# Kernel optimization log

Measured on AMD Instinct MI355X. Metric: run time of the kernel, lower is better.

The kernel has to match this reference:

```python
import jax, jax.numpy as jnp
import numpy as np

B, S, D, H, DK, DV, DO = 2, 2048, 1024, 16, 64, 64, 1024


def setup_inputs() -> dict:
    key = jax.random.key(0)
    k0, k1, k2, k3, k4 = jax.random.split(key, 5)
    x = jax.random.normal(k0, (B, S, D), dtype=jnp.float32)
    # Stacked per-head projection weights (original uses H separate Linear(bias=False));
    # stored as [H, D, d_head] so q = x @ Wq[h] per head.
    Wq = jax.random.normal(k1, (H, D, DK), dtype=jnp.float32) * 0.02
    Wk = jax.random.normal(k2, (H, D, DK), dtype=jnp.float32) * 0.02
    Wv = jax.random.normal(k3, (H, D, DV), dtype=jnp.float32) * 0.02
    # Output projection Linear(dim_v*num_heads, dim_out, bias=False), stored [H*DV, DO]
    Wo = jax.random.normal(k4, (H * DV, DO), dtype=jnp.float32) * 0.02
    return {"x": x, "Wq": Wq, "Wk": Wk, "Wv": Wv, "Wo": Wo}


def reference(x, Wq, Wk, Wv, Wo):
    # Cross-head batched version of the per-head Python loop (same math).
    q = jnp.einsum('bsd,hde->bhse', x, Wq)  # [B,H,S,DK]
    k = jnp.einsum('bsd,hde->bhse', x, Wk)  # [B,H,S,DK]
    v = jnp.einsum('bsd,hde->bhse', x, Wv)  # [B,H,S,DV]
    scale = 1.0 / jnp.sqrt(jnp.asarray(k.shape[-1], dtype=x.dtype))
    scores = jnp.einsum('bhqe,bhke->bhqk', q, k) * scale  # [B,H,S,S]
    attn = jax.nn.softmax(scores, axis=-1)
    o = jnp.einsum('bhqk,bhke->bhqe', attn, v)  # [B,H,S,DV]
    # concat heads along feature dim (head order preserved)
    o = jnp.transpose(o, (0, 2, 1, 3)).reshape(o.shape[0], o.shape[2], -1)  # [B,S,H*DV]
    return o @ Wo  # [B,S,DO]
```

## Files before the change

### kernel.cpp

```cpp
#include <hip/hip_runtime.h>

typedef __bf16 bf16;
typedef __attribute__((ext_vector_type(8))) short short8;
typedef __attribute__((ext_vector_type(4))) short short4v;
typedef __attribute__((ext_vector_type(4))) float floatx4;

#define DEVINL __device__ __forceinline__

DEVINL void gll16(const void* g, void* l) {
  __builtin_amdgcn_global_load_lds((const __attribute__((address_space(1))) void*)g,
                                   (__attribute__((address_space(3))) void*)l, 16, 0, 0);
}

DEVINL float fast_exp2(float x) { return __builtin_amdgcn_exp2f(x); }

#define QSCALE 0.18033688011112042f

__global__ __launch_bounds__(256) void prep_all(const float* __restrict__ x,
                                                const float* __restrict__ Wq,
                                                const float* __restrict__ Wk,
                                                const float* __restrict__ Wv,
                                                const float* __restrict__ Wo,
                                                bf16* __restrict__ x_bf,
                                                bf16* __restrict__ WbigT,
                                                bf16* __restrict__ WoT) {
  __shared__ float tile[64][65];
  int bid = blockIdx.x;
  if (bid < 2048) {
    int i = (bid * 256 + threadIdx.x) * 8;
    float4 a = *(const float4*)(x + i);
    float4 b = *(const float4*)(x + i + 4);
    union { bf16 h[8]; short8 s; } u;
    u.h[0] = (bf16)a.x; u.h[1] = (bf16)a.y; u.h[2] = (bf16)a.z; u.h[3] = (bf16)a.w;
    u.h[4] = (bf16)b.x; u.h[5] = (bf16)b.y; u.h[6] = (bf16)b.z; u.h[7] = (bf16)b.w;
    *(short8*)(x_bf + i) = u.s;
    return;
  }
  int t = bid - 2048;
  int which = t >> 8;
  t &= 255;
  const float* in;
  bf16* out;
  int C, tilesC, tilesPerBatch;
  long inStride;
  if (which < 3) {
    in = which == 0 ? Wq : (which == 1 ? Wk : Wv);
    out = WbigT + (long)which * 1024 * 1024;
    C = 64; tilesC = 1; tilesPerBatch = 16; inStride = 65536;
  } else {
    in = Wo; out = WoT;
    C = 1024; tilesC = 16; tilesPerBatch = 256; inStride = 0;
  }
  int batch = t / tilesPerBatch;
  int tt = t % tilesPerBatch;
  int ri = tt / tilesC, ci = tt % tilesC;
  const float* src = in + batch * inStride;
  bf16* dst = out + batch * (long)65536 * (which < 3 ? 1 : 0);
  int tx = threadIdx.x & 63, ty = threadIdx.x >> 6;
#pragma unroll
  for (int i = 0; i < 16; i++) {
    int r = ty + i * 4;
    tile[r][tx] = src[(long)(ri * 64 + r) * C + ci * 64 + tx];
  }
  __syncthreads();
#pragma unroll
  for (int i = 0; i < 16; i++) {
    int c = ty + i * 4;
    dst[(long)(ci * 64 + c) * 1024 + ri * 64 + tx] = (bf16)tile[tx][c];
  }
}

__global__ __launch_bounds__(512, 2) void gemm256_qkv(const bf16* __restrict__ A,
                                                      const bf16* __restrict__ BT,
                                                      bf16* __restrict__ q_ws,
                                                      bf16* __restrict__ k_ws,
                                                      bf16* __restrict__ v_ws) {
  extern __shared__ char lds[];
  int swz = (blockIdx.x & 7) * 24 + (blockIdx.x >> 3);
  int bm = swz / 12, bn = swz % 12;
  int tid = threadIdx.x, lane = tid & 63, wid = tid >> 6;
  int wm = wid >> 2, wn = wid & 3;
  int ql = lane & 15, g = lane >> 4;
  int sw = (ql & 7) << 4;
  int hB = wn >> 1;
  char* ldsA = lds;
  char* ldsB = lds + 65536;

  const char* Abase = (const char*)A + (long)bm * 256 * 2048;
  const char* Bbase = (const char*)BT + (long)bn * 256 * 2048;
  int scb = ((tid & 7) * 16) ^ (((tid >> 3) & 7) << 4);

  floatx4 acc[8][4] = {};
  short8 aF[4], bF[4];

#define STG(dst0, src0, kt_, h_) do {                                              \
    _Pragma("unroll") for (int j_ = 0; j_ < 2; j_++)                               \
      gll16((src0) + (long)((h_) * 128 + j_ * 64 + (tid >> 3)) * 2048              \
                   + (kt_) * 128 + scb,                                            \
            (dst0) + ((kt_) & 1) * 32768 + (h_) * 16384 + j_ * 8192 + wid * 1024); \
  } while (0)
#define LDA(slot_, frh_, kk_) do {                                                 \
    _Pragma("unroll") for (int j_ = 0; j_ < 4; j_++)                               \
      aF[j_] = *(const short8*)(ldsA + (slot_) * 32768 + wm * 16384 +              \
               (((frh_) * 4 + j_) * 16 + ql) * 128 + (((kk_) * 64 + g * 16) ^ sw));\
  } while (0)
#define LDB(slot_, kk_) do {                                                       \
    _Pragma("unroll") for (int f_ = 0; f_ < 4; f_++)                               \
      bF[f_] = *(const short8*)(ldsB + (slot_) * 32768 + hB * 16384 +              \
               ((wn & 1) * 64 + f_ * 16 + ql) * 128 + (((kk_) * 64 + g * 16) ^ sw));\
  } while (0)
#define MFMA16(frh_) do {                                                          \
    __builtin_amdgcn_s_setprio(1);                                                 \
    _Pragma("unroll") for (int j_ = 0; j_ < 4; j_++)                               \
      _Pragma("unroll") for (int f_ = 0; f_ < 4; f_++)                             \
        acc[(frh_) * 4 + j_][f_] = __builtin_amdgcn_mfma_f32_16x16x32_bf16(        \
            aF[j_], bF[f_], acc[(frh_) * 4 + j_][f_], 0, 0, 0);                    \
    __builtin_amdgcn_s_setprio(0);                                                 \
  } while (0)
#define BAR __builtin_amdgcn_s_barrier()
#define LG0 asm volatile("s_waitcnt lgkmcnt(0)" ::: "memory")

  STG(ldsB, Bbase, 0, 0); STG(ldsB, Bbase, 0, 1);
  STG(ldsA, Abase, 0, 0); STG(ldsA, Abase, 0, 1);
  STG(ldsB, Bbase, 1, 0);

  for (int it = 0; it < 8; it++) {
    int b1 = 2 * it + 1, a2 = 2 * it + 2, b2 = 2 * it + 3;
    bool more = it < 7;
    asm volatile("s_waitcnt vmcnt(2)" ::: "memory");
    BAR;
    LDA(0, 0, 0); LDB(0, 0);
    STG(ldsA, Abase, b1, 0);
    BAR; LG0; MFMA16(0); BAR;
    LDA(0, 1, 0);
    STG(ldsA, Abase, b1, 1);
    BAR; LG0; MFMA16(1); BAR;
    LDA(0, 0, 1); LDB(0, 1);
    STG(ldsB, Bbase, b1, 1);
    BAR; LG0; MFMA16(0); BAR;
    LDA(0, 1, 1);
    if (more) STG(ldsB, Bbase, a2, 0);
    BAR; LG0; MFMA16(1); BAR;
    if (more) { asm volatile("s_waitcnt vmcnt(2)" ::: "memory"); }
    else      { asm volatile("s_waitcnt vmcnt(0)" ::: "memory"); }
    BAR;
    LDA(1, 0, 0); LDB(1, 0);
    if (more) STG(ldsB, Bbase, a2, 1);
    BAR; LG0; MFMA16(0); BAR;
    LDA(1, 1, 0);
    if (more) STG(ldsA, Abase, a2, 0);
    BAR; LG0; MFMA16(1); BAR;
    LDA(1, 0, 1); LDB(1, 1);
    if (more) STG(ldsA, Abase, a2, 1);
    BAR; LG0; MFMA16(0); BAR;
    LDA(1, 1, 1);
    if (more) STG(ldsB, Bbase, b2, 0);
    BAR; LG0; MFMA16(1); BAR;
  }
#undef STG
#undef LDA
#undef LDB
#undef MFMA16
#undef BAR
#undef LG0

  if (bn < 8) {
    bf16* dst = (bn < 4) ? q_ws : k_ws;
    float scale = (bn < 4) ? QSCALE : 1.0f;
#pragma unroll
    for (int fr = 0; fr < 8; fr++)
#pragma unroll
      for (int fc = 0; fc < 4; fc++)
#pragma unroll
        for (int i = 0; i < 4; i++) {
          int r = bm * 256 + wm * 128 + fr * 16 + g * 4 + i;
          int c = bn * 256 + wn * 64 + fc * 16 + ql;
          int b = r >> 11, s = r & 2047;
          int h = (c >> 6) & 15, e = c & 63;
          long bh = (long)b * 16 + h;
          dst[(bh * 2048 + s) * 64 + e] = (bf16)(acc[fr][fc][i] * scale);
        }
  } else {
#pragma unroll
    for (int fr = 0; fr < 8; fr++)
#pragma unroll
      for (int fc = 0; fc < 4; fc++) {
        int local_c = wn * 64 + fc * 16 + ql;
        int ls0 = wm * 128 + fr * 16 + g * 4;
        int s6 = ls0 & 63;
        int sp = (ls0 & ~63) | (s6 & 35) | ((s6 & 12) << 1) | ((s6 & 16) >> 2);
        union { bf16 hh[4]; short4v s4; } u;
#pragma unroll
        for (int i = 0; i < 4; i++) u.hh[i] = (bf16)acc[fr][fc][i];
        *(short4v*)(lds + local_c * 512 + ((sp * 2) ^ ((local_c & 7) << 4))) = u.s4;
      }
    __syncthreads();
    int b = bm >> 3;
    long sbase = (long)(bm & 7) * 256;
#pragma unroll
    for (int j = 0; j < 16; j++) {
      int local_c = wid * 32 + j * 2 + (lane >> 5);
      int chunk = lane & 31;
      int cg = bn * 256 + local_c;
      int h = (cg >> 6) & 15, e = cg & 63;
      long bh = (long)b * 16 + h;
      char* dstp = (char*)v_ws + ((bh * 64 + e) * 2048 + sbase) * 2 + chunk * 16;
      *(short8*)dstp = *(const short8*)(lds + local_c * 512 + ((chunk * 16) ^ ((local_c & 7) << 4)));
    }
  }
}

__global__ __launch_bounds__(256) void gemm_out(const bf16* __restrict__ A,
                                                const bf16* __restrict__ BT,
                                                float* __restrict__ Cout,
                                                int N, int gridN) {
  int cpx = gridDim.x >> 3;
  int swz = (blockIdx.x & 7) * cpx + (blockIdx.x >> 3);
  int bm = swz / gridN, bn = swz % gridN;
  __shared__ char lds[65536];
  int tid = threadIdx.x;
  int lane = tid & 63, wid = tid >> 6;
  int wr = wid >> 1, wc = wid & 1;
  floatx4 acc[4][4] = {};
  const char* Abase = (const char*)A + (long)bm * 128 * 2048;
  const char* Bbase = (const char*)BT + (long)bn * 128 * 2048;
  int scb = ((tid & 7) * 16) ^ (((tid >> 3) & 7) << 4);

#define OSTG(kt_) do {                                                             \
    char* la_ = lds + ((kt_) & 1) * 16384;                                         \
    char* lb_ = lds + 32768 + ((kt_) & 1) * 16384;                                 \
    _Pragma("unroll") for (int q_ = 0; q_ < 4; q_++) {                             \
      gll16(Abase + (long)(q_ * 32 + (tid >> 3)) * 2048 + (kt_) * 128 + scb,       \
            la_ + q_ * 4096 + wid * 1024);                                         \
      gll16(Bbase + (long)(q_ * 32 + (tid >> 3)) * 2048 + (kt_) * 128 + scb,       \
            lb_ + q_ * 4096 + wid * 1024);                                         \
    }                                                                              \
  } while (0)

  OSTG(0);
  for (int kt = 0; kt < 16; kt++) {
    if (kt < 15) {
      OSTG(kt + 1);
      asm volatile("s_waitcnt vmcnt(8)" ::: "memory");
    } else {
      asm volatile("s_waitcnt vmcnt(0)" ::: "memory");
    }
    __builtin_amdgcn_s_barrier();
    char* la = lds + (kt & 1) * 16384;
    char* lb = lds + 32768 + (kt & 1) * 16384;
#pragma unroll
    for (int kk = 0; kk < 2; kk++) {
      short8 a[4], b[4];
#pragma unroll
      for (int mi = 0; mi < 4; mi++) {
        int row = wr * 64 + mi * 16 + (lane & 15);
        int col = (kk * 64 + (lane >> 4) * 16) ^ ((row & 7) << 4);
        a[mi] = *(const short8*)(la + row * 128 + col);
      }
#pragma unroll
      for (int ni = 0; ni < 4; ni++) {
        int row = wc * 64 + ni * 16 + (lane & 15);
        int col = (kk * 64 + (lane >> 4) * 16) ^ ((row & 7) << 4);
        b[ni] = *(const short8*)(lb + row * 128 + col);
      }
#pragma unroll
      for (int mi = 0; mi < 4; mi++)
#pragma unroll
        for (int ni = 0; ni < 4; ni++)
          acc[mi][ni] = __builtin_amdgcn_mfma_f32_16x16x32_bf16(a[mi], b[ni], acc[mi][ni], 0, 0, 0);
    }
    __builtin_amdgcn_s_barrier();
  }
#undef OSTG

#pragma unroll
  for (int mi = 0; mi < 4; mi++)
#pragma unroll
    for (int ni = 0; ni < 4; ni++)
#pragma unroll
      for (int i = 0; i < 4; i++) {
        int r = bm * 128 + wr * 64 + mi * 16 + (lane >> 4) * 4 + i;
        int c = bn * 128 + wc * 64 + ni * 16 + (lane & 15);
        Cout[(long)r * N + c] = acc[mi][ni][i];
      }
}

__global__ __launch_bounds__(1024, 4) void attn_kernel(const bf16* __restrict__ q_ws,
                                                       const bf16* __restrict__ k_ws,
                                                       const bf16* __restrict__ v_ws,
                                                       bf16* __restrict__ obuf) {
  extern __shared__ char lds[];
  int wgid = ((blockIdx.x & 7) << 5) + (blockIdx.x >> 3);
  int qt = wgid & 7;
  int bh = wgid >> 3;
  int b = bh >> 4, h = bh & 15;
  int tid = threadIdx.x, lane = tid & 63, wid = tid >> 6;
  int grp = wid >> 3, w8 = wid & 7;
  int ql = lane & 15, g = lane >> 4;
  char* kbuf = lds + grp * 65536;
  char* vbuf = kbuf + 32768;

  const char* kbase = (const char*)k_ws + (long)bh * 2048 * 128 + (long)grp * 16 * 64 * 128;
  const char* vbase = (const char*)v_ws + (long)bh * 64 * 4096 + (long)grp * 16 * 128;

  int srow = w8 * 8 + (lane >> 3);
  int scb = ((lane & 7) * 16) ^ (((lane >> 3) & 7) << 4);

#define STAGE(t_) do {                                                              \
    gll16(kbase + ((long)(t_) * 64 + srow) * 128 + scb,                             \
          kbuf + ((t_) & 3) * 8192 + w8 * 1024);                                    \
    gll16(vbase + (long)srow * 4096 + (long)(t_) * 128 + scb,                       \
          vbuf + ((t_) & 3) * 8192 + w8 * 1024);                                    \
  } while (0)

#define WAIT2_BAR do {                                                              \
    asm volatile("s_waitcnt vmcnt(2)" ::: "memory");                                \
    __builtin_amdgcn_s_barrier();                                                   \
    asm volatile("" ::: "memory");                                                  \
  } while (0)

  int sw = (ql & 7) << 4;
  int fof0 = ql * 128 + ((g * 16) ^ sw);
  int fof1 = ql * 128 + ((64 + g * 16) ^ sw);

  const bf16* qrowL = q_ws + ((long)bh * 2048 + qt * 256 + w8 * 32 + ql) * 64 + 8 * g;
  short8 qL0 = *(const short8*)(qrowL);
  short8 qL1 = *(const short8*)(qrowL + 32);
  short8 qH0 = *(const short8*)(qrowL + 1024);
  short8 qH1 = *(const short8*)(qrowL + 1024 + 32);

  union { bf16 hh[8]; short8 s; } uo1;
#pragma unroll
  for (int i = 0; i < 8; i++) uo1.hh[i] = (bf16)1.0f;
  const short8 ones = uo1.s;

  floatx4 lL = {}, lH = {};
  floatx4 oL[4] = {}, oH[4] = {};
  floatx4 saL[4], saH[4];
  short8 pbL[2], pbH[2];

#define QKSTEP(kc) do {                                                             \
    __builtin_amdgcn_s_setprio(1);                                                  \
    _Pragma("unroll") for (int t_ = 0; t_ < 4; t_++) {                              \
      short8 kf = *(const short8*)((kc) + fof0 + t_ * 2048);                        \
      saL[t_] = __builtin_amdgcn_mfma_f32_16x16x32_bf16(kf, qL0, (floatx4){}, 0, 0, 0); \
      saH[t_] = __builtin_amdgcn_mfma_f32_16x16x32_bf16(kf, qH0, (floatx4){}, 0, 0, 0); \
    }                                                                               \
    _Pragma("unroll") for (int t_ = 0; t_ < 4; t_++) {                              \
      short8 kf = *(const short8*)((kc) + fof1 + t_ * 2048);                        \
      saL[t_] = __builtin_amdgcn_mfma_f32_16x16x32_bf16(kf, qL1, saL[t_], 0, 0, 0); \
      saH[t_] = __builtin_amdgcn_mfma_f32_16x16x32_bf16(kf, qH1, saH[t_], 0, 0, 0); \
    }                                                                               \
    __builtin_amdgcn_s_setprio(0);                                                  \
  } while (0)

#define SM_HALF(sa, pb, l_acc, o_acc) do {                                          \
    if (__builtin_expect(l_acc[0] > 1e30f, 0)) {                                    \
      const float c_ = 7.8886091e-31f;                                  \
      _Pragma("unroll") for (int t_ = 0; t_ < 4; t_++)                              \
        _Pragma("unroll") for (int i_ = 0; i_ < 4; i_++) o_acc[t_][i_] *= c_;       \
      _Pragma("unroll") for (int i_ = 0; i_ < 4; i_++) l_acc[i_] *= c_;             \
    }                                                                               \
    _Pragma("unroll") for (int kk_ = 0; kk_ < 2; kk_++) {                           \
      union { bf16 hh[8]; short8 s; } up_;                                          \
      _Pragma("unroll") for (int r_ = 0; r_ < 4; r_++)                              \
        up_.hh[r_] = (bf16)fast_exp2(sa[2 * kk_][r_]);                              \
      _Pragma("unroll") for (int r_ = 0; r_ < 4; r_++)                              \
        up_.hh[4 + r_] = (bf16)fast_exp2(sa[2 * kk_ + 1][r_]);                      \
      pb[kk_] = up_.s;                                                              \
    }                                                                               \
  } while (0)

#define SMSTEP do { SM_HALF(saL, pbL, lL, oL); SM_HALF(saH, pbH, lH, oH); } while (0)

#define PVSTEP(vc) do {                                                             \
    __builtin_amdgcn_s_setprio(1);                                                  \
    lL = __builtin_amdgcn_mfma_f32_16x16x32_bf16(ones, pbL[0], lL, 0, 0, 0);        \
    lL = __builtin_amdgcn_mfma_f32_16x16x32_bf16(ones, pbL[1], lL, 0, 0, 0);        \
    lH = __builtin_amdgcn_mfma_f32_16x16x32_bf16(ones, pbH[0], lH, 0, 0, 0);        \
    lH = __builtin_amdgcn_mfma_f32_16x16x32_bf16(ones, pbH[1], lH, 0, 0, 0);        \
    _Pragma("unroll") for (int t_ = 0; t_ < 4; t_++) {                              \
      short8 vf = *(const short8*)((vc) + fof0 + t_ * 2048);                        \
      oL[t_] = __builtin_amdgcn_mfma_f32_16x16x32_bf16(vf, pbL[0], oL[t_], 0, 0, 0);\
      oH[t_] = __builtin_amdgcn_mfma_f32_16x16x32_bf16(vf, pbH[0], oH[t_], 0, 0, 0);\
    }                                                                               \
    _Pragma("unroll") for (int t_ = 0; t_ < 4; t_++) {                              \
      short8 vf = *(const short8*)((vc) + fof1 + t_ * 2048);                        \
      oL[t_] = __builtin_amdgcn_mfma_f32_16x16x32_bf16(vf, pbL[1], oL[t_], 0, 0, 0);\
      oH[t_] = __builtin_amdgcn_mfma_f32_16x16x32_bf16(vf, pbH[1], oH[t_], 0, 0, 0);\
    }                                                                               \
    __builtin_amdgcn_s_setprio(0);                                                  \
  } while (0)

  STAGE(0); STAGE(1);
  WAIT2_BAR;
  QKSTEP(kbuf + 0 * 8192);
  STAGE(2);
  SMSTEP;
  WAIT2_BAR;
  STAGE(3);
  QKSTEP(kbuf + 1 * 8192);

  for (int t = 1; t <= 13; t++) {
    PVSTEP(vbuf + ((t - 1) & 3) * 8192);
    SMSTEP;
    WAIT2_BAR;
    if (t <= 12) STAGE(t + 3);
    QKSTEP(kbuf + ((t + 1) & 3) * 8192);
  }

  PVSTEP(vbuf + (13 & 3) * 8192);
  SMSTEP;
  __syncthreads();
  QKSTEP(kbuf + (15 & 3) * 8192);

  PVSTEP(vbuf + (14 & 3) * 8192);
  SMSTEP;
  PVSTEP(vbuf + (15 & 3) * 8192);

#undef STAGE
#undef WAIT2_BAR
#undef QKSTEP
#undef SM_HALF
#undef SMSTEP
#undef PVSTEP

  __syncthreads();
  if (grp == 1) {
    char* pbase = lds + 65536 + w8 * 8192;
#pragma unroll
    for (int t = 0; t < 4; t++) {
      *(floatx4*)(pbase + (t * 2 + 0) * 1024 + lane * 16) = oL[t];
      *(floatx4*)(pbase + (t * 2 + 1) * 1024 + lane * 16) = oH[t];
    }
    *(float2*)(lds + w8 * 512 + lane * 8) = make_float2(lL[0], lH[0]);
  }
  __syncthreads();
  if (grp == 0) {
    float2 lp = *(const float2*)(lds + w8 * 512 + lane * 8);
    const char* pbase = lds + 65536 + w8 * 8192;
    float invL = 1.f / (lL[0] + lp.x);
    float invH = 1.f / (lH[0] + lp.y);
    int s = qt * 256 + w8 * 32 + ql;
    bf16* orowL = obuf + ((long)b * 2048 + s) * 1024 + h * 64;
    bf16* orowH = orowL + 16 * 1024;
#pragma unroll
    for (int t = 0; t < 4; t++) {
      floatx4 aL = *(const floatx4*)(pbase + (t * 2 + 0) * 1024 + lane * 16);
      floatx4 aH = *(const floatx4*)(pbase + (t * 2 + 1) * 1024 + lane * 16);
      union { bf16 hh[4]; short4v s4; } uo;
#pragma unroll
      for (int r = 0; r < 4; r++) uo.hh[r] = (bf16)((oL[t][r] + aL[r]) * invL);
      *(short4v*)(orowL + t * 16 + 4 * g) = uo.s4;
#pragma unroll
      for (int r = 0; r < 4; r++) uo.hh[r] = (bf16)((oH[t][r] + aH[r]) * invH);
      *(short4v*)(orowH + t * 16 + 4 * g) = uo.s4;
    }
  }
}

extern "C" void kernel_launch(void* const* d_in, const int* in_sizes, int n_in,
                              void* d_out, int out_size, void* d_ws, size_t ws_size,
                              hipStream_t stream) {
  const float* x  = (const float*)d_in[0];
  const float* Wq = (const float*)d_in[1];
  const float* Wk = (const float*)d_in[2];
  const float* Wv = (const float*)d_in[3];
  const float* Wo = (const float*)d_in[4];
  float* out = (float*)d_out;

  char* ws = (char*)d_ws;
  bf16* x_bf  = (bf16*)(ws);
  bf16* WbigT = (bf16*)(ws + 8388608);
  bf16* WoT   = (bf16*)(ws + 14680064);
  bf16* q_ws  = (bf16*)(ws + 16777216);
  bf16* k_ws  = (bf16*)(ws + 25165824);
  bf16* v_ws  = (bf16*)(ws + 33554432);
  bf16* obuf  = (bf16*)(ws + 41943040);

  hipFuncSetAttribute((const void*)gemm256_qkv,
                      hipFuncAttributeMaxDynamicSharedMemorySize, 131072);
  hipFuncSetAttribute((const void*)attn_kernel,
                      hipFuncAttributeMaxDynamicSharedMemorySize, 131072);

  prep_all<<<3072, 256, 0, stream>>>(x, Wq, Wk, Wv, Wo, x_bf, WbigT, WoT);
  gemm256_qkv<<<192, 512, 131072, stream>>>(x_bf, WbigT, q_ws, k_ws, v_ws);
  attn_kernel<<<256, 1024, 131072, stream>>>(q_ws, k_ws, v_ws, obuf);
  gemm_out<<<256, 256, 0, stream>>>(obuf, WoT, out, 1024, 8);
}
```

Baseline: 100.3 us.

## Switch attention kernel to 32x32x16 MFMA tiles with VALU row-sum accumulation

Rewrites the attention inner loop to use 32x32x16 bf16 MFMAs instead of 16x16x32, with a matching change to the V-layout permutation in the projection epilogue. The softmax denominator is now summed with VALU adds during exponentiation instead of extra MFMAs against a ones vector. The software pipeline order is also changed to softmax, then PV, then barrier, stage, QK. The goal is fewer MFMA issues and less register and LDS-fragment overhead per tile. In exchange it uses larger accumulator registers and a more complex lane mapping, with some correctness risk in the layout permutation.

```diff
diff --git a/kernel.cpp b/kernel.cpp
--- a/kernel.cpp
+++ b/kernel.cpp
@@ -4,6 +4,7 @@
 typedef __attribute__((ext_vector_type(8))) short short8;
 typedef __attribute__((ext_vector_type(4))) short short4v;
 typedef __attribute__((ext_vector_type(4))) float floatx4;
+typedef __attribute__((ext_vector_type(16))) float floatx16;
 
 #define DEVINL __device__ __forceinline__
 
@@ -187,8 +188,7 @@
       for (int fc = 0; fc < 4; fc++) {
         int local_c = wn * 64 + fc * 16 + ql;
         int ls0 = wm * 128 + fr * 16 + g * 4;
-        int s6 = ls0 & 63;
-        int sp = (ls0 & ~63) | (s6 & 35) | ((s6 & 12) << 1) | ((s6 & 16) >> 2);
+        int sp = (ls0 & ~12) | ((ls0 & 4) << 1) | ((ls0 & 8) >> 1);
         union { bf16 hh[4]; short4v s4; } u;
 #pragma unroll
         for (int i = 0; i < 4; i++) u.hh[i] = (bf16)acc[fr][fc][i];
@@ -293,15 +293,15 @@
   int wgid = ((blockIdx.x & 7) << 5) + (blockIdx.x >> 3);
   int qt = wgid & 7;
   int bh = wgid >> 3;
-  int b = bh >> 4, h = bh & 15;
+  int b = bh >> 4, hh = bh & 15;
   int tid = threadIdx.x, lane = tid & 63, wid = tid >> 6;
   int grp = wid >> 3, w8 = wid & 7;
-  int ql = lane & 15, g = lane >> 4;
+  int l31 = lane & 31, h2 = lane >> 5;
   char* kbuf = lds + grp * 65536;
   char* vbuf = kbuf + 32768;
 
-  const char* kbase = (const char*)k_ws + (long)bh * 2048 * 128 + (long)grp * 16 * 64 * 128;
-  const char* vbase = (const char*)v_ws + (long)bh * 64 * 4096 + (long)grp * 16 * 128;
+  const char* kbase = (const char*)k_ws + (long)bh * 2048 * 128 + (long)grp * 131072;
+  const char* vbase = (const char*)v_ws + (long)bh * 64 * 4096 + (long)grp * 2048;
 
   int srow = w8 * 8 + (lane >> 3);
   int scb = ((lane & 7) * 16) ^ (((lane >> 3) & 7) << 4);
@@ -319,75 +319,66 @@
     asm volatile("" ::: "memory");                                                  \
   } while (0)
 
-  int sw = (ql & 7) << 4;
-  int fof0 = ql * 128 + ((g * 16) ^ sw);
-  int fof1 = ql * 128 + ((64 + g * 16) ^ sw);
-
-  const bf16* qrowL = q_ws + ((long)bh * 2048 + qt * 256 + w8 * 32 + ql) * 64 + 8 * g;
-  short8 qL0 = *(const short8*)(qrowL);
-  short8 qL1 = *(const short8*)(qrowL + 32);
-  short8 qH0 = *(const short8*)(qrowL + 1024);
-  short8 qH1 = *(const short8*)(qrowL + 1024 + 32);
-
-  union { bf16 hh[8]; short8 s; } uo1;
-#pragma unroll
-  for (int i = 0; i < 8; i++) uo1.hh[i] = (bf16)1.0f;
-  const short8 ones = uo1.s;
-
-  floatx4 lL = {}, lH = {};
-  floatx4 oL[4] = {}, oH[4] = {};
-  floatx4 saL[4], saH[4];
-  short8 pbL[2], pbH[2];
+  int rofs = l31 * 128, swz = (lane & 7) << 4, h16 = h2 << 4;
+  int fof[4];
+#pragma unroll
+  for (int m = 0; m < 4; m++) fof[m] = rofs + ((32 * m + h16) ^ swz);
+
+  const bf16* qrow = q_ws + ((long)bh * 2048 + qt * 256 + w8 * 32 + l31) * 64 + 8 * h2;
+  short8 qreg[4];
+#pragma unroll
+  for (int dt = 0; dt < 4; dt++) qreg[dt] = *(const short8*)(qrow + 16 * dt);
+
+  floatx16 sa0, sa1;
+  floatx16 o0 = {}, o1 = {};
+  short8 pb[4];
+  float ls[4] = {0.f, 0.f, 0.f, 0.f};
 
 #define QKSTEP(kc) do {                                                             \
     __builtin_amdgcn_s_setprio(1);                                                  \
-    _Pragma("unroll") for (int t_ = 0; t_ < 4; t_++) {                              \
-      short8 kf = *(const short8*)((kc) + fof0 + t_ * 2048);                        \
-      saL[t_] = __builtin_amdgcn_mfma_f32_16x16x32_bf16(kf, qL0, (floatx4){}, 0, 0, 0); \
-      saH[t_] = __builtin_amdgcn_mfma_f32_16x16x32_bf16(kf, qH0, (floatx4){}, 0, 0, 0); \
-    }                                                                               \
-    _Pragma("unroll") for (int t_ = 0; t_ < 4; t_++) {                              \
-      short8 kf = *(const short8*)((kc) + fof1 + t_ * 2048);                        \
-      saL[t_] = __builtin_amdgcn_mfma_f32_16x16x32_bf16(kf, qL1, saL[t_], 0, 0, 0); \
-      saH[t_] = __builtin_amdgcn_mfma_f32_16x16x32_bf16(kf, qH1, saH[t_], 0, 0, 0); \
+    _Pragma("unroll") for (int dt_ = 0; dt_ < 4; dt_++) {                           \
+      short8 ka_ = *(const short8*)((kc) + fof[dt_]);                               \
+      short8 kb_ = *(const short8*)((kc) + 4096 + fof[dt_]);                        \
+      if (dt_ == 0) {                                                               \
+        sa0 = __builtin_amdgcn_mfma_f32_32x32x16_bf16(ka_, qreg[0], (floatx16){}, 0, 0, 0); \
+        sa1 = __builtin_amdgcn_mfma_f32_32x32x16_bf16(kb_, qreg[0], (floatx16){}, 0, 0, 0); \
+      } else {                                                                      \
+        sa0 = __builtin_amdgcn_mfma_f32_32x32x16_bf16(ka_, qreg[dt_], sa0, 0, 0, 0);\
+        sa1 = __builtin_amdgcn_mfma_f32_32x32x16_bf16(kb_, qreg[dt_], sa1, 0, 0, 0);\
+      }                                                                             \
     }                                                                               \
     __builtin_amdgcn_s_setprio(0);                                                  \
   } while (0)
 
-#define SM_HALF(sa, pb, l_acc, o_acc) do {                                          \
-    if (__builtin_expect(l_acc[0] > 1e30f, 0)) {                                    \
+#define SMSTEP do {                                                                 \
+    if (__builtin_expect(ls[0] > 1e30f, 0)) {                                       \
       const float c_ = 7.8886091e-31f;                                  \
-      _Pragma("unroll") for (int t_ = 0; t_ < 4; t_++)                              \
-        _Pragma("unroll") for (int i_ = 0; i_ < 4; i_++) o_acc[t_][i_] *= c_;       \
-      _Pragma("unroll") for (int i_ = 0; i_ < 4; i_++) l_acc[i_] *= c_;             \
+      _Pragma("unroll") for (int i_ = 0; i_ < 4; i_++) ls[i_] *= c_;                \
+      _Pragma("unroll") for (int i_ = 0; i_ < 16; i_++) { o0[i_] *= c_; o1[i_] *= c_; } \
     }                                                                               \
-    _Pragma("unroll") for (int kk_ = 0; kk_ < 2; kk_++) {                           \
-      union { bf16 hh[8]; short8 s; } up_;                                          \
-      _Pragma("unroll") for (int r_ = 0; r_ < 4; r_++)                              \
-        up_.hh[r_] = (bf16)fast_exp2(sa[2 * kk_][r_]);                              \
-      _Pragma("unroll") for (int r_ = 0; r_ < 4; r_++)                              \
-        up_.hh[4 + r_] = (bf16)fast_exp2(sa[2 * kk_ + 1][r_]);                      \
-      pb[kk_] = up_.s;                                                              \
+    { union { bf16 hh_[8]; short8 s_; } u_;                                         \
+      _Pragma("unroll") for (int j_ = 0; j_ < 8; j_++) {                            \
+        float e_ = fast_exp2(sa0[j_]); ls[j_ & 3] += e_; u_.hh_[j_] = (bf16)e_; }   \
+      pb[0] = u_.s_;                                                                \
+      _Pragma("unroll") for (int j_ = 0; j_ < 8; j_++) {                            \
+        float e_ = fast_exp2(sa0[8 + j_]); ls[j_ & 3] += e_; u_.hh_[j_] = (bf16)e_; } \
+      pb[1] = u_.s_;                                                                \
+      _Pragma("unroll") for (int j_ = 0; j_ < 8; j_++) {                            \
+        float e_ = fast_exp2(sa1[j_]); ls[j_ & 3] += e_; u_.hh_[j_] = (bf16)e_; }   \
+      pb[2] = u_.s_;                                                                \
+      _Pragma("unroll") for (int j_ = 0; j_ < 8; j_++) {                            \
+        float e_ = fast_exp2(sa1[8 + j_]); ls[j_ & 3] += e_; u_.hh_[j_] = (bf16)e_; } \
+      pb[3] = u_.s_;                                                                \
     }                                                                               \
   } while (0)
-
-#define SMSTEP do { SM_HALF(saL, pbL, lL, oL); SM_HALF(saH, pbH, lH, oH); } while (0)
 
 #define PVSTEP(vc) do {                                                             \
     __builtin_amdgcn_s_setprio(1);                                                  \
-    lL = __builtin_amdgcn_mfma_f32_16x16x32_bf16(ones, pbL[0], lL, 0, 0, 0);        \
-    lL = __builtin_amdgcn_mfma_f32_16x16x32_bf16(ones, pbL[1], lL, 0, 0, 0);        \
-    lH = __builtin_amdgcn_mfma_f32_16x16x32_bf16(ones, pbH[0], lH, 0, 0, 0);        \
-    lH = __builtin_amdgcn_mfma_f32_16x16x32_bf16(ones, pbH[1], lH, 0, 0, 0);        \
-    _Pragma("unroll") for (int t_ = 0; t_ < 4; t_++) {                              \
-      short8 vf = *(const short8*)((vc) + fof0 + t_ * 2048);                        \
-      oL[t_] = __builtin_amdgcn_mfma_f32_16x16x32_bf16(vf, pbL[0], oL[t_], 0, 0, 0);\
-      oH[t_] = __builtin_amdgcn_mfma_f32_16x16x32_bf16(vf, pbH[0], oH[t_], 0, 0, 0);\
-    }                                                                               \
-    _Pragma("unroll") for (int t_ = 0; t_ < 4; t_++) {                              \
-      short8 vf = *(const short8*)((vc) + fof1 + t_ * 2048);                        \
-      oL[t_] = __builtin_amdgcn_mfma_f32_16x16x32_bf16(vf, pbL[1], oL[t_], 0, 0, 0);\
-      oH[t_] = __builtin_amdgcn_mfma_f32_16x16x32_bf16(vf, pbH[1], oH[t_], 0, 0, 0);\
+    _Pragma("unroll") for (int c_ = 0; c_ < 4; c_++) {                              \
+      short8 va_ = *(const short8*)((vc) + fof[c_]);                                \
+      short8 vb_ = *(const short8*)((vc) + 4096 + fof[c_]);                         \
+      o0 = __builtin_amdgcn_mfma_f32_32x32x16_bf16(va_, pb[c_], o0, 0, 0, 0);       \
+      o1 = __builtin_amdgcn_mfma_f32_32x32x16_bf16(vb_, pb[c_], o1, 0, 0, 0);       \
     }                                                                               \
     __builtin_amdgcn_s_setprio(0);                                                  \
   } while (0)
@@ -396,65 +387,59 @@
   WAIT2_BAR;
   QKSTEP(kbuf + 0 * 8192);
   STAGE(2);
+
+  for (int t = 0; t <= 12; t++) {
+    SMSTEP;
+    PVSTEP(vbuf + (t & 3) * 8192);
+    WAIT2_BAR;
+    STAGE(t + 3);
+    QKSTEP(kbuf + ((t + 1) & 3) * 8192);
+  }
   SMSTEP;
+  PVSTEP(vbuf + (13 & 3) * 8192);
   WAIT2_BAR;
-  STAGE(3);
-  QKSTEP(kbuf + 1 * 8192);
-
-  for (int t = 1; t <= 13; t++) {
-    PVSTEP(vbuf + ((t - 1) & 3) * 8192);
-    SMSTEP;
-    WAIT2_BAR;
-    if (t <= 12) STAGE(t + 3);
-    QKSTEP(kbuf + ((t + 1) & 3) * 8192);
-  }
-
-  PVSTEP(vbuf + (13 & 3) * 8192);
+  QKSTEP(kbuf + (14 & 3) * 8192);
   SMSTEP;
-  __syncthreads();
+  PVSTEP(vbuf + (14 & 3) * 8192);
+  asm volatile("s_waitcnt vmcnt(0)" ::: "memory");
+  __builtin_amdgcn_s_barrier();
   QKSTEP(kbuf + (15 & 3) * 8192);
-
-  PVSTEP(vbuf + (14 & 3) * 8192);
   SMSTEP;
   PVSTEP(vbuf + (15 & 3) * 8192);
 
 #undef STAGE
 #undef WAIT2_BAR
 #undef QKSTEP
-#undef SM_HALF
 #undef SMSTEP
 #undef PVSTEP
 
   __syncthreads();
+  float lsum = (ls[0] + ls[1]) + (ls[2] + ls[3]);
+  float lpair = lsum + __shfl_xor(lsum, 32);
+  int sq = qt * 256 + w8 * 32 + l31;
   if (grp == 1) {
-    char* pbase = lds + 65536 + w8 * 8192;
-#pragma unroll
-    for (int t = 0; t < 4; t++) {
-      *(floatx4*)(pbase + (t * 2 + 0) * 1024 + lane * 16) = oL[t];
-      *(floatx4*)(pbase + (t * 2 + 1) * 1024 + lane * 16) = oH[t];
-    }
-    *(float2*)(lds + w8 * 512 + lane * 8) = make_float2(lL[0], lH[0]);
+    char* pk = lds + 65536 + w8 * 8192;
+    *(floatx16*)(pk + lane * 64) = o0;
+    *(floatx16*)(pk + 4096 + lane * 64) = o1;
+    if (h2 == 0) *(float*)(lds + (w8 * 32 + l31) * 4) = lpair;
   }
   __syncthreads();
   if (grp == 0) {
-    float2 lp = *(const float2*)(lds + w8 * 512 + lane * 8);
-    const char* pbase = lds + 65536 + w8 * 8192;
-    float invL = 1.f / (lL[0] + lp.x);
-    float invH = 1.f / (lH[0] + lp.y);
-    int s = qt * 256 + w8 * 32 + ql;
-    bf16* orowL = obuf + ((long)b * 2048 + s) * 1024 + h * 64;
-    bf16* orowH = orowL + 16 * 1024;
-#pragma unroll
-    for (int t = 0; t < 4; t++) {
-      floatx4 aL = *(const floatx4*)(pbase + (t * 2 + 0) * 1024 + lane * 16);
-      floatx4 aH = *(const floatx4*)(pbase + (t * 2 + 1) * 1024 + lane * 16);
-      union { bf16 hh[4]; short4v s4; } uo;
-#pragma unroll
-      for (int r = 0; r < 4; r++) uo.hh[r] = (bf16)((oL[t][r] + aL[r]) * invL);
-      *(short4v*)(orowL + t * 16 + 4 * g) = uo.s4;
-#pragma unroll
-      for (int r = 0; r < 4; r++) uo.hh[r] = (bf16)((oH[t][r] + aH[r]) * invH);
-      *(short4v*)(orowH + t * 16 + 4 * g) = uo.s4;
+    const char* pk = lds + 65536 + w8 * 8192;
+    floatx16 a0 = *(const floatx16*)(pk + lane * 64);
+    floatx16 a1 = *(const floatx16*)(pk + 4096 + lane * 64);
+    float lp = *(const float*)(lds + (w8 * 32 + l31) * 4);
+    float inv = 1.f / (lpair + lp);
+    bf16* orow = obuf + ((long)b * 2048 + sq) * 1024 + hh * 64;
+#pragma unroll
+    for (int rg = 0; rg < 4; rg++) {
+      union { bf16 hv[4]; short4v s4; } uo;
+#pragma unroll
+      for (int i = 0; i < 4; i++) uo.hv[i] = (bf16)((o0[4 * rg + i] + a0[4 * rg + i]) * inv);
+      *(short4v*)(orow + 8 * rg + 4 * h2) = uo.s4;
+#pragma unroll
+      for (int i = 0; i < 4; i++) uo.hv[i] = (bf16)((o1[4 * rg + i] + a1[4 * rg + i]) * inv);
+      *(short4v*)(orow + 32 + 8 * rg + 4 * h2) = uo.s4;
     }
   }
 }
```

New measurement: 111.9 us. +11.6%, slower.
